# Performance work log

Measured on AMD Instinct MI355X. Metric: run time of the kernel, lower is better.

Reference implementation:

```python
import jax, jax.numpy as jnp
import numpy as np

B, C, V, D = 1024, 10, 50257, 128
EPS = 1e-3  # floor so log(decoded) is finite


def setup_inputs() -> dict:
    key = jax.random.key(0)
    k1, k2, k3, k4, k5, k6 = jax.random.split(key, 6)
    context = jax.random.randint(k1, (B, C), 0, V)
    mu_lambda = jax.random.normal(k2, (B, D), dtype=jnp.float32)
    sigma_lambda = jax.random.uniform(k3, (B, D), dtype=jnp.float32, minval=EPS, maxval=1.0)
    mu_x = jax.random.normal(k4, (B, 1, D), dtype=jnp.float32)
    sigma_x = jax.random.uniform(k5, (B, 1, D), dtype=jnp.float32, minval=EPS, maxval=1.0)
    decoded = jax.random.uniform(k6, (B, V), dtype=jnp.float32, minval=EPS, maxval=1.0)
    return {"context": context, "mu_lambda": mu_lambda, "sigma_lambda": sigma_lambda,
            "mu_x": mu_x, "sigma_x": sigma_x, "decoded": decoded}


def reference(context, mu_lambda, sigma_lambda, mu_x, sigma_x, decoded):
    # log-likelihood: gather decoded probs at context word ids, log, sum over [B, C]
    probs = jnp.take_along_axis(decoded, context, axis=1)  # [B, C]
    ll = jnp.sum(jnp.log(probs))
    # KL between N(mu_lambda, sigma_lambda^2) and prior N(mu_x, sigma_x^2), elementwise over [B, D]
    mu_x2 = mu_x[:, 0, :]      # [B, D]
    sig_x2 = sigma_x[:, 0, :]  # [B, D]
    kl = (jnp.log(sig_x2 / sigma_lambda)
          + (sigma_lambda ** 2 + (mu_lambda - mu_x2) ** 2) / (2.0 * sig_x2 ** 2)
          - 0.5)
    return -ll + jnp.sum(kl)
```

## Files before the change

### kernel.cpp

```cpp
#include <hip/hip_runtime.h>
#include <hip/hip_bf16.h>


#define B_ 1024
#define C_ 10
#define V_ 50257
#define D_ 128

__global__ __launch_bounds__(256) void elbo_kernel(
    const int* __restrict__ context,
    const float* __restrict__ mu_l,
    const float* __restrict__ sig_l,
    const float* __restrict__ mu_x,
    const float* __restrict__ sig_x,
    const float* __restrict__ decoded,
    float* __restrict__ out)
{
    const int tid = blockIdx.x * blockDim.x + threadIdx.x;
    const int nth = gridDim.x * blockDim.x;

    float local = 0.0f;

    for (int i = tid; i < B_ * D_; i += nth) {
        float ml = mu_l[i];
        float sl = sig_l[i];
        float mx = mu_x[i];
        float sx = sig_x[i];
        float diff = ml - mx;
        local += __logf(sx / sl) + (sl * sl + diff * diff) / (2.0f * sx * sx) - 0.5f;
    }

    for (int i = tid; i < B_ * C_; i += nth) {
        int b = i / C_;
        int idx = context[i];
        local -= __logf(decoded[(size_t)b * V_ + idx]);
    }

    for (int off = 32; off > 0; off >>= 1)
        local += __shfl_down(local, off, 64);

    __shared__ float wsum[4];
    int lane = threadIdx.x & 63;
    int wid  = threadIdx.x >> 6;
    if (lane == 0) wsum[wid] = local;
    __syncthreads();

    if (threadIdx.x == 0)
        atomicAdd(out, wsum[0] + wsum[1] + wsum[2] + wsum[3]);
}

extern "C" void kernel_launch(void* const* d_in, const int* in_sizes, int n_in,
                              void* d_out, int out_size, void* d_ws, size_t ws_size,
                              hipStream_t stream) {
    const int*   context = (const int*)  d_in[0];
    const float* mu_l    = (const float*)d_in[1];
    const float* sig_l   = (const float*)d_in[2];
    const float* mu_x    = (const float*)d_in[3];
    const float* sig_x   = (const float*)d_in[4];
    const float* decoded = (const float*)d_in[5];
    float* out = (float*)d_out;

    hipMemsetAsync(out, 0, sizeof(float), stream);

    elbo_kernel<<<256, 256, 0, stream>>>(context, mu_l, sig_l, mu_x, sig_x,
                                         decoded, out);
}
```

Before: 245.1 us.

## Vectorize KL loads with float4 and replace atomic reduction with two-stage reduce

Each thread now loads one float4 from each KL input and handles at most one context gather, with no grid-stride loops. Block partials go to a workspace, and a second single-block kernel sums them, replacing the memset and the atomicAdd. This is meant to cut memory transactions and the cost of the memset and atomic, at the price of a second kernel launch and a hardcoded grid size.

```diff
diff --git a/kernel.cpp b/kernel.cpp
--- a/kernel.cpp
+++ b/kernel.cpp
@@ -6,33 +6,37 @@
 #define C_ 10
 #define V_ 50257
 #define D_ 128
+#define NB1 128
 
-__global__ __launch_bounds__(256) void elbo_kernel(
+__global__ __launch_bounds__(256) void elbo_partial(
     const int* __restrict__ context,
-    const float* __restrict__ mu_l,
-    const float* __restrict__ sig_l,
-    const float* __restrict__ mu_x,
-    const float* __restrict__ sig_x,
+    const float4* __restrict__ mu_l,
+    const float4* __restrict__ sig_l,
+    const float4* __restrict__ mu_x,
+    const float4* __restrict__ sig_x,
     const float* __restrict__ decoded,
-    float* __restrict__ out)
+    float* __restrict__ partial)
 {
-    const int tid = blockIdx.x * blockDim.x + threadIdx.x;
-    const int nth = gridDim.x * blockDim.x;
+    const int tid = blockIdx.x * 256 + threadIdx.x;
 
-    float local = 0.0f;
+    float4 ml = mu_l[tid];
+    float4 sl = sig_l[tid];
+    float4 mx = mu_x[tid];
+    float4 sx = sig_x[tid];
 
-    for (int i = tid; i < B_ * D_; i += nth) {
-        float ml = mu_l[i];
-        float sl = sig_l[i];
-        float mx = mu_x[i];
-        float sx = sig_x[i];
-        float diff = ml - mx;
-        local += __logf(sx / sl) + (sl * sl + diff * diff) / (2.0f * sx * sx) - 0.5f;
+    float local;
+    {
+        float d0 = ml.x - mx.x, d1 = ml.y - mx.y, d2 = ml.z - mx.z, d3 = ml.w - mx.w;
+        float t0 = __logf(sx.x / sl.x) + (sl.x * sl.x + d0 * d0) / (2.0f * sx.x * sx.x) - 0.5f;
+        float t1 = __logf(sx.y / sl.y) + (sl.y * sl.y + d1 * d1) / (2.0f * sx.y * sx.y) - 0.5f;
+        float t2 = __logf(sx.z / sl.z) + (sl.z * sl.z + d2 * d2) / (2.0f * sx.z * sx.z) - 0.5f;
+        float t3 = __logf(sx.w / sl.w) + (sl.w * sl.w + d3 * d3) / (2.0f * sx.w * sx.w) - 0.5f;
+        local = (t0 + t1) + (t2 + t3);
     }
 
-    for (int i = tid; i < B_ * C_; i += nth) {
-        int b = i / C_;
-        int idx = context[i];
+    if (tid < B_ * C_) {
+        int b = tid / C_;
+        int idx = context[tid];
         local -= __logf(decoded[(size_t)b * V_ + idx]);
     }
 
@@ -46,22 +50,38 @@
     __syncthreads();
 
     if (threadIdx.x == 0)
-        atomicAdd(out, wsum[0] + wsum[1] + wsum[2] + wsum[3]);
+        partial[blockIdx.x] = (wsum[0] + wsum[1]) + (wsum[2] + wsum[3]);
+}
+
+__global__ __launch_bounds__(128) void elbo_final(
+    const float* __restrict__ partial,
+    float* __restrict__ out)
+{
+    float local = partial[threadIdx.x];
+    for (int off = 32; off > 0; off >>= 1)
+        local += __shfl_down(local, off, 64);
+
+    __shared__ float wsum[2];
+    if ((threadIdx.x & 63) == 0) wsum[threadIdx.x >> 6] = local;
+    __syncthreads();
+
+    if (threadIdx.x == 0)
+        out[0] = wsum[0] + wsum[1];
 }
 
 extern "C" void kernel_launch(void* const* d_in, const int* in_sizes, int n_in,
                               void* d_out, int out_size, void* d_ws, size_t ws_size,
                               hipStream_t stream) {
-    const int*   context = (const int*)  d_in[0];
-    const float* mu_l    = (const float*)d_in[1];
-    const float* sig_l   = (const float*)d_in[2];
-    const float* mu_x    = (const float*)d_in[3];
-    const float* sig_x   = (const float*)d_in[4];
-    const float* decoded = (const float*)d_in[5];
-    float* out = (float*)d_out;
+    const int*    context = (const int*)   d_in[0];
+    const float4* mu_l    = (const float4*)d_in[1];
+    const float4* sig_l   = (const float4*)d_in[2];
+    const float4* mu_x    = (const float4*)d_in[3];
+    const float4* sig_x   = (const float4*)d_in[4];
+    const float*  decoded = (const float*) d_in[5];
+    float* partial = (float*)d_ws;
+    float* out     = (float*)d_out;
 
-    hipMemsetAsync(out, 0, sizeof(float), stream);
-
-    elbo_kernel<<<256, 256, 0, stream>>>(context, mu_l, sig_l, mu_x, sig_x,
-                                         decoded, out);
+    elbo_partial<<<NB1, 256, 0, stream>>>(context, mu_l, sig_l, mu_x, sig_x,
+                                          decoded, partial);
+    elbo_final<<<1, 128, 0, stream>>>(partial, out);
 }
```

Result: no change. 242.9 us (-0.9%).
